# Kernel optimization log

Measured on AMD Instinct MI355X. Metric: run time of the kernel, lower is better.

The kernel has to match this reference:

```python
import jax, jax.numpy as jnp
import numpy as np

# NF4 codebook (bitsandbytes nf4 data type, 16 levels)
NF4_TABLE = np.array([
    -1.0, -0.6961928009986877, -0.5250730514526367, -0.39491748809814453,
    -0.28444138169288635, -0.18477343022823334, -0.09105003625154495, 0.0,
    0.07958029955625534, 0.16093020141124725, 0.24611230194568634,
    0.33791524171829224, 0.44070982933044434, 0.5626170039176941,
    0.7229568362236023, 1.0], dtype=np.float32)

BLOCKSIZE = 64
SCALING = 32.0 / 16.0  # lora_alpha / r


def setup_inputs() -> dict:
    key = jax.random.key(0)
    k1, k2, k3, k4, k5 = jax.random.split(key, 5)
    tokens, in_f, out_f, r = 256, 4096, 11008, 16
    x = jax.random.normal(k1, (tokens, in_f), dtype=jnp.float32)
    q_codes = jax.random.randint(k2, (out_f, in_f), 0, 16, dtype=jnp.int32)
    absmax = jax.random.uniform(k3, (out_f, in_f // BLOCKSIZE), dtype=jnp.float32)
    lora_A = jax.random.normal(k4, (r, in_f), dtype=jnp.float32) * (1.0 / np.sqrt(in_f))
    lora_B = jax.random.normal(k5, (out_f, r), dtype=jnp.float32) * 0.02
    return {"x": x, "q_codes": q_codes, "absmax": absmax,
            "lora_A": lora_A, "lora_B": lora_B}


def reference(x, q_codes, absmax, lora_A, lora_B):
    out_f, in_f = q_codes.shape
    nf4 = jnp.asarray(NF4_TABLE, dtype=x.dtype)
    # Dequantize: codebook lookup, then per-block absmax scale.
    W = nf4[q_codes].reshape(out_f, in_f // BLOCKSIZE, BLOCKSIZE)
    W = (W * absmax[:, :, None]).reshape(out_f, in_f)  # [out_f, in_f]
    # Base 4-bit linear (no bias in bnb Linear4bit default here).
    base = x @ W.T  # [tokens, out_f]
    # LoRA path: dropout p=0 is identity in eval; scaling = alpha/r.
    lora = (x @ lora_A.T) @ lora_B.T  # [tokens, r] -> [tokens, out_f]
    return base + lora * jnp.asarray(SCALING, dtype=x.dtype)
```

## Files before the change

kernel.cpp:

```cpp
#include <hip/hip_runtime.h>
#include <hip/hip_fp16.h>

typedef unsigned int uint;
typedef unsigned short ushort;

typedef __attribute__((ext_vector_type(8))) _Float16 f16x8;
typedef __attribute__((ext_vector_type(4))) float f32x4;

#define TOK 256
#define OUTF 11008
#define INF 4096
#define BM 256
#define BN 64
#define NT2 172
#define NWT 11008

__device__ __constant__ float NF4_TBL[16] = {
    -1.0f, -0.6961928009986877f, -0.5250730514526367f, -0.39491748809814453f,
    -0.28444138169288635f, -0.18477343022823334f, -0.09105003625154495f, 0.0f,
    0.07958029955625534f, 0.16093020141124725f, 0.24611230194568634f,
    0.33791524171829224f, 0.44070982933044434f, 0.5626170039176941f,
    0.7229568362236023f, 1.0f};

__device__ __forceinline__ ushort f2h(float f) {
  return __half_as_ushort(__float2half(f));
}

__device__ __forceinline__ float nf4v(int c, int tbits) {
  return __int_as_float(__builtin_amdgcn_ds_bpermute(c << 2, tbits));
}

__device__ __forceinline__ uint2 dq4(int4 c, __half2 ax2, int tbits) {
  __half2 h0 = __floats2half2_rn(nf4v(c.x, tbits), nf4v(c.y, tbits));
  __half2 h1 = __floats2half2_rn(nf4v(c.z, tbits), nf4v(c.w, tbits));
  h0 = __hmul2(h0, ax2);
  h1 = __hmul2(h1, ax2);
  union { __half2 h[2]; uint2 u; } r;
  r.h[0] = h0; r.h[1] = h1;
  return r.u;
}

__global__ __launch_bounds__(256)
void prep_kernel(const int* __restrict__ qc, const float* __restrict__ am,
                 uint4* __restrict__ wf4, const float* __restrict__ x,
                 uint4* __restrict__ xf4, const float4* __restrict__ lB4,
                 ushort4* __restrict__ lBh4) {
  const int tid = threadIdx.x;
  if (blockIdx.x < NWT) {
    const int b = blockIdx.x;
    const int g = b >> 6, kb = b & 63;
    const int r = tid >> 2;
    const int c = tid & 3;
    const int n = g * 64 + r;
    const int tbits = __float_as_int(NF4_TBL[tid & 15]);
    const __half2 ax2 = __float2half2_rn(am[(size_t)n * 64 + kb]);
    const int4* src = (const int4*)(qc + (size_t)n * INF + kb * 64 + c * 16);
    int4 q0 = src[0], q1 = src[1], q2 = src[2], q3 = src[3];
    uint2 d0 = dq4(q0, ax2, tbits), d1 = dq4(q1, ax2, tbits);
    uint2 d2 = dq4(q2, ax2, tbits), d3 = dq4(q3, ax2, tbits);
    const int rlo = r & 15, nt = r >> 4;
    const int i8a = c * 2, i8b = c * 2 + 1;
    uint4* dst = wf4 + (size_t)b * 512;
    dst[((i8a & 3) * 16 + rlo) * 8 + (i8a >> 2) * 4 + nt] = (uint4){d0.x, d0.y, d1.x, d1.y};
    dst[((i8b & 3) * 16 + rlo) * 8 + (i8b >> 2) * 4 + nt] = (uint4){d2.x, d2.y, d3.x, d3.y};
  } else {
    const int stride = 256 * 256;
    const int t0 = (blockIdx.x - NWT) * 256 + tid;
    for (int f = t0; f < TOK * INF / 8; f += stride) {
      int l = f & 63;
      int rlo = l & 15, chunk = l >> 4;
      int ms = (f >> 6) & 7;
      int mt = ms >> 1, ks2 = ms & 1;
      int w = (f >> 9) & 3;
      int kb = f >> 11;
      int m = w * 64 + mt * 16 + rlo;
      int k0 = kb * 64 + (ks2 * 4 + chunk) * 8;
      const float4* src = (const float4*)(x + (size_t)m * INF + k0);
      float4 v0 = src[0], v1 = src[1];
      union { ushort4 h[2]; uint4 u; } pk;
      pk.h[0].x = f2h(v0.x); pk.h[0].y = f2h(v0.y); pk.h[0].z = f2h(v0.z); pk.h[0].w = f2h(v0.w);
      pk.h[1].x = f2h(v1.x); pk.h[1].y = f2h(v1.y); pk.h[1].z = f2h(v1.z); pk.h[1].w = f2h(v1.w);
      xf4[f] = pk.u;
    }
    for (int i = t0; i < OUTF * 16; i += stride) {
      int n = i >> 4, jq = i & 15;
      ushort4 o = {0, 0, 0, 0};
      if (jq < 4) {
        float4 v = lB4[n * 4 + jq];
        o.x = f2h(v.x); o.y = f2h(v.y); o.z = f2h(v.z); o.w = f2h(v.w);
      }
      lBh4[i] = o;
    }
  }
}

__global__ __launch_bounds__(1024)
void xa_kernel(const float* __restrict__ x, const float* __restrict__ lA,
               ushort* __restrict__ xa2) {
  const int m = blockIdx.x;
  const int t = threadIdx.x;
  const float4* x4 = (const float4*)(x + (size_t)m * INF);
  const float4* lA4 = (const float4*)lA;
  float4 xv = x4[t];
  float acc[16];
#pragma unroll
  for (int j = 0; j < 16; ++j) {
    float4 a = lA4[j * (INF / 4) + t];
    acc[j] = xv.x * a.x + xv.y * a.y + xv.z * a.z + xv.w * a.w;
  }
#pragma unroll
  for (int j = 0; j < 16; ++j)
#pragma unroll
    for (int s = 32; s > 0; s >>= 1) acc[j] += __shfl_xor(acc[j], s, 64);
  __shared__ float red[16][16];
  const int w = t >> 6, l = t & 63;
  if (l == 0) {
#pragma unroll
    for (int j = 0; j < 16; ++j) red[w][j] = acc[j];
  }
  __syncthreads();
  if (t < 64) {
    ushort v = 0;
    if (t < 16) {
      float s = 0.f;
#pragma unroll
      for (int w2 = 0; w2 < 16; ++w2) s += red[w2][t];
      v = f2h(2.0f * s);
    }
    xa2[m * 64 + t] = v;
  }
}

__global__ __launch_bounds__(256, 2)
void gemm_kernel(const ushort* __restrict__ wf, const ushort* __restrict__ xf,
                 const ushort* __restrict__ lBh, const ushort* __restrict__ xa2,
                 float* __restrict__ dest32, ushort* __restrict__ dest16,
                 int nst, int fp16out) {
  const int tid = threadIdx.x;
  const int w = tid >> 6;
  const int l = tid & 63;
  const int chunk = l >> 4;
  const int rlo = l & 15;
  const int split = blockIdx.x / NT2;
  const int ntile = blockIdx.x - split * NT2;
  const int n0 = ntile * BN;
  const int kb0 = split * nst;

  f32x4 acc[4][4];
#pragma unroll
  for (int mt = 0; mt < 4; ++mt)
#pragma unroll
    for (int nt = 0; nt < 4; ++nt) acc[mt][nt] = (f32x4){0.f, 0.f, 0.f, 0.f};

  auto loadA = [&](f16x8 ar[8], int kb) {
    const ushort* base = xf + ((size_t)kb * 4 + w) * 4096 + l * 8;
#pragma unroll
    for (int i = 0; i < 8; ++i) ar[i] = *(const f16x8*)(base + i * 512);
  };
  auto loadB = [&](f16x8 br[8], int kb) {
    const ushort* base = wf + (size_t)(ntile * 64 + kb) * 4096 + l * 64;
#pragma unroll
    for (int f = 0; f < 8; ++f) br[f] = *(const f16x8*)(base + f * 8);
  };
  auto compute = [&](f16x8 ar[8], f16x8 br[8]) {
    __builtin_amdgcn_s_setprio(1);
#pragma unroll
    for (int ks2 = 0; ks2 < 2; ++ks2)
#pragma unroll
      for (int mt = 0; mt < 4; ++mt)
#pragma unroll
        for (int nt = 0; nt < 4; ++nt)
          acc[mt][nt] = __builtin_amdgcn_mfma_f32_16x16x32_f16(
              ar[mt * 2 + ks2], br[ks2 * 4 + nt], acc[mt][nt], 0, 0, 0);
    __builtin_amdgcn_s_setprio(0);
  };

  f16x8 aA[8], bA[8], aB[8], bB[8];
  loadB(bA, kb0);
  loadA(aA, kb0);
  loadB(bB, kb0 + 1);
  loadA(aB, kb0 + 1);

  for (int s = 0; s < nst; s += 2) {
    compute(aA, bA);
    if (s + 2 < nst) { loadB(bA, kb0 + s + 2); loadA(aA, kb0 + s + 2); }
    compute(aB, bB);
    if (s + 3 < nst) { loadB(bB, kb0 + s + 3); loadA(aB, kb0 + s + 3); }
  }

  if (split == 0) {
    f16x8 a_l[4], b_l[4];
#pragma unroll
    for (int mt = 0; mt < 4; ++mt)
      a_l[mt] = *(const f16x8*)(xa2 + (size_t)(w * 64 + mt * 16 + rlo) * 64 + chunk * 8);
#pragma unroll
    for (int nt = 0; nt < 4; ++nt)
      b_l[nt] = *(const f16x8*)(lBh + (size_t)(n0 + nt * 16 + rlo) * 64 + chunk * 8);
#pragma unroll
    for (int mt = 0; mt < 4; ++mt)
#pragma unroll
      for (int nt = 0; nt < 4; ++nt)
        acc[mt][nt] = __builtin_amdgcn_mfma_f32_16x16x32_f16(a_l[mt], b_l[nt], acc[mt][nt], 0, 0, 0);
  }

  if (fp16out) {
    ushort* dst = dest16 + (size_t)split * TOK * OUTF;
#pragma unroll
    for (int mt = 0; mt < 4; ++mt) {
#pragma unroll
      for (int nt = 0; nt < 4; ++nt) {
        int c = n0 + nt * 16 + rlo;
#pragma unroll
        for (int r = 0; r < 4; ++r) {
          int row = w * 64 + mt * 16 + chunk * 4 + r;
          dst[(size_t)row * OUTF + c] = f2h(acc[mt][nt][r]);
        }
      }
    }
  } else {
    float* dst = dest32;
#pragma unroll
    for (int mt = 0; mt < 4; ++mt) {
#pragma unroll
      for (int nt = 0; nt < 4; ++nt) {
        int c = n0 + nt * 16 + rlo;
#pragma unroll
        for (int r = 0; r < 4; ++r) {
          int row = w * 64 + mt * 16 + chunk * 4 + r;
          dst[(size_t)row * OUTF + c] = acc[mt][nt][r];
        }
      }
    }
  }
}

__global__ void reduce_kernel(const uint4* __restrict__ part, float4* __restrict__ out,
                              int ks) {
  const int QN8 = TOK * OUTF / 8;
  int i = blockIdx.x * blockDim.x + threadIdx.x;
  if (i < QN8) {
    float s0 = 0.f, s1 = 0.f, s2 = 0.f, s3 = 0.f, s4 = 0.f, s5 = 0.f, s6 = 0.f, s7 = 0.f;
    for (int sp = 0; sp < ks; ++sp) {
      uint4 v = part[(size_t)sp * QN8 + i];
      union { uint u; __half2 h; } a, b, c, d;
      a.u = v.x; b.u = v.y; c.u = v.z; d.u = v.w;
      float2 fa = __half22float2(a.h), fb = __half22float2(b.h);
      float2 fc = __half22float2(c.h), fd = __half22float2(d.h);
      s0 += fa.x; s1 += fa.y; s2 += fb.x; s3 += fb.y;
      s4 += fc.x; s5 += fc.y; s6 += fd.x; s7 += fd.y;
    }
    out[2 * i] = (float4){s0, s1, s2, s3};
    out[2 * i + 1] = (float4){s4, s5, s6, s7};
  }
}

extern "C" void kernel_launch(void* const* d_in, const int* in_sizes, int n_in,
                              void* d_out, int out_size, void* d_ws, size_t ws_size,
                              hipStream_t stream) {
  const float* x = (const float*)d_in[0];
  const int* qc = (const int*)d_in[1];
  const float* am = (const float*)d_in[2];
  const float* lA = (const float*)d_in[3];
  const float* lB = (const float*)d_in[4];
  float* out = (float*)d_out;

  const size_t off_lB = (size_t)TOK * INF * 2;
  const size_t off_xa2 = off_lB + (size_t)OUTF * 64 * 2;
  const size_t off_wf = off_xa2 + (size_t)TOK * 64 * 2;
  const size_t off_part = off_wf + (size_t)NWT * 8192;
  const size_t part_bytes = (size_t)TOK * OUTF * 2;

  ushort* xf = (ushort*)d_ws;
  ushort* lBh = (ushort*)((char*)d_ws + off_lB);
  ushort* xa2 = (ushort*)((char*)d_ws + off_xa2);
  ushort* wf = (ushort*)((char*)d_ws + off_wf);
  ushort* part = (ushort*)((char*)d_ws + off_part);

  int ks = 1;
  if (ws_size >= off_part + 8 * part_bytes) ks = 8;
  else if (ws_size >= off_part + 4 * part_bytes) ks = 4;
  else if (ws_size >= off_part + 2 * part_bytes) ks = 2;
  const int fp16out = (ks > 1) ? 1 : 0;

  prep_kernel<<<NWT + 256, 256, 0, stream>>>(qc, am, (uint4*)wf, x, (uint4*)xf,
                                             (const float4*)lB, (ushort4*)lBh);
  xa_kernel<<<TOK, 1024, 0, stream>>>(x, lA, xa2);
  gemm_kernel<<<NT2 * ks, 256, 0, stream>>>(wf, xf, lBh, xa2, out, part,
                                            64 / ks, fp16out);
  if (ks > 1)
    reduce_kernel<<<(TOK * OUTF / 8 + 255) / 256, 256, 0, stream>>>((const uint4*)part,
                                                                    (float4*)out, ks);
}
```

Before: 359.5 us.

## Fuse NF4 dequantization into GEMM and drop the fp16 weight buffer

Removes the separate pass that dequantized NF4 codes into a pre-laid-out fp16 weight buffer. The GEMM now loads int32 codes and absmax directly and dequantizes with ds_bpermute in registers. Each wave now owns a 16-column strip across all 256 tokens instead of a 64x64 tile. This is meant to avoid writing and re-reading the intermediate weight buffer. In exchange, activation fragments are re-read from global/L2 by every wave and dequantization ALU work sits inside the MFMA loop.

```diff
diff --git a/kernel.cpp b/kernel.cpp
--- a/kernel.cpp
+++ b/kernel.cpp
@@ -10,10 +10,8 @@
 #define TOK 256
 #define OUTF 11008
 #define INF 4096
-#define BM 256
 #define BN 64
 #define NT2 172
-#define NWT 11008
 
 __device__ __constant__ float NF4_TBL[16] = {
     -1.0f, -0.6961928009986877f, -0.5250730514526367f, -0.39491748809814453f,
@@ -40,57 +38,34 @@
   return r.u;
 }
 
-__global__ __launch_bounds__(256)
-void prep_kernel(const int* __restrict__ qc, const float* __restrict__ am,
-                 uint4* __restrict__ wf4, const float* __restrict__ x,
-                 uint4* __restrict__ xf4, const float4* __restrict__ lB4,
-                 ushort4* __restrict__ lBh4) {
-  const int tid = threadIdx.x;
-  if (blockIdx.x < NWT) {
-    const int b = blockIdx.x;
-    const int g = b >> 6, kb = b & 63;
-    const int r = tid >> 2;
-    const int c = tid & 3;
-    const int n = g * 64 + r;
-    const int tbits = __float_as_int(NF4_TBL[tid & 15]);
-    const __half2 ax2 = __float2half2_rn(am[(size_t)n * 64 + kb]);
-    const int4* src = (const int4*)(qc + (size_t)n * INF + kb * 64 + c * 16);
-    int4 q0 = src[0], q1 = src[1], q2 = src[2], q3 = src[3];
-    uint2 d0 = dq4(q0, ax2, tbits), d1 = dq4(q1, ax2, tbits);
-    uint2 d2 = dq4(q2, ax2, tbits), d3 = dq4(q3, ax2, tbits);
-    const int rlo = r & 15, nt = r >> 4;
-    const int i8a = c * 2, i8b = c * 2 + 1;
-    uint4* dst = wf4 + (size_t)b * 512;
-    dst[((i8a & 3) * 16 + rlo) * 8 + (i8a >> 2) * 4 + nt] = (uint4){d0.x, d0.y, d1.x, d1.y};
-    dst[((i8b & 3) * 16 + rlo) * 8 + (i8b >> 2) * 4 + nt] = (uint4){d2.x, d2.y, d3.x, d3.y};
-  } else {
-    const int stride = 256 * 256;
-    const int t0 = (blockIdx.x - NWT) * 256 + tid;
-    for (int f = t0; f < TOK * INF / 8; f += stride) {
-      int l = f & 63;
-      int rlo = l & 15, chunk = l >> 4;
-      int ms = (f >> 6) & 7;
-      int mt = ms >> 1, ks2 = ms & 1;
-      int w = (f >> 9) & 3;
-      int kb = f >> 11;
-      int m = w * 64 + mt * 16 + rlo;
-      int k0 = kb * 64 + (ks2 * 4 + chunk) * 8;
-      const float4* src = (const float4*)(x + (size_t)m * INF + k0);
-      float4 v0 = src[0], v1 = src[1];
-      union { ushort4 h[2]; uint4 u; } pk;
-      pk.h[0].x = f2h(v0.x); pk.h[0].y = f2h(v0.y); pk.h[0].z = f2h(v0.z); pk.h[0].w = f2h(v0.w);
-      pk.h[1].x = f2h(v1.x); pk.h[1].y = f2h(v1.y); pk.h[1].z = f2h(v1.z); pk.h[1].w = f2h(v1.w);
-      xf4[f] = pk.u;
-    }
-    for (int i = t0; i < OUTF * 16; i += stride) {
-      int n = i >> 4, jq = i & 15;
-      ushort4 o = {0, 0, 0, 0};
-      if (jq < 4) {
-        float4 v = lB4[n * 4 + jq];
-        o.x = f2h(v.x); o.y = f2h(v.y); o.z = f2h(v.z); o.w = f2h(v.w);
-      }
-      lBh4[i] = o;
-    }
+__global__ void prep_kernel(const float* __restrict__ x, uint4* __restrict__ xf4,
+                            const float4* __restrict__ lB4, ushort4* __restrict__ lBh4) {
+  const int stride = gridDim.x * blockDim.x;
+  const int t0 = blockIdx.x * blockDim.x + threadIdx.x;
+  for (int f = t0; f < TOK * INF / 8; f += stride) {
+    int l = f & 63;
+    int rlo = l & 15, chunk = l >> 4;
+    int ms = (f >> 6) & 7;
+    int mt = ms >> 1, ks2 = ms & 1;
+    int m64 = (f >> 9) & 3;
+    int kb = f >> 11;
+    int m = m64 * 64 + mt * 16 + rlo;
+    int k0 = kb * 64 + (ks2 * 4 + chunk) * 8;
+    const float4* src = (const float4*)(x + (size_t)m * INF + k0);
+    float4 v0 = src[0], v1 = src[1];
+    union { ushort4 h[2]; uint4 u; } pk;
+    pk.h[0].x = f2h(v0.x); pk.h[0].y = f2h(v0.y); pk.h[0].z = f2h(v0.z); pk.h[0].w = f2h(v0.w);
+    pk.h[1].x = f2h(v1.x); pk.h[1].y = f2h(v1.y); pk.h[1].z = f2h(v1.z); pk.h[1].w = f2h(v1.w);
+    xf4[f] = pk.u;
+  }
+  for (int i = t0; i < OUTF * 16; i += stride) {
+    int n = i >> 4, jq = i & 15;
+    ushort4 o = {0, 0, 0, 0};
+    if (jq < 4) {
+      float4 v = lB4[n * 4 + jq];
+      o.x = f2h(v.x); o.y = f2h(v.y); o.z = f2h(v.z); o.w = f2h(v.w);
+    }
+    lBh4[i] = o;
   }
 }
 
@@ -132,10 +107,10 @@
 }
 
 __global__ __launch_bounds__(256, 2)
-void gemm_kernel(const ushort* __restrict__ wf, const ushort* __restrict__ xf,
-                 const ushort* __restrict__ lBh, const ushort* __restrict__ xa2,
-                 float* __restrict__ dest32, ushort* __restrict__ dest16,
-                 int nst, int fp16out) {
+void gemm_kernel(const int* __restrict__ qc, const float* __restrict__ am,
+                 const ushort* __restrict__ xf, const ushort* __restrict__ lBh,
+                 const ushort* __restrict__ xa2, float* __restrict__ dest32,
+                 ushort* __restrict__ dest16, int nst, int fp16out) {
   const int tid = threadIdx.x;
   const int w = tid >> 6;
   const int l = tid & 63;
@@ -143,94 +118,90 @@
   const int rlo = l & 15;
   const int split = blockIdx.x / NT2;
   const int ntile = blockIdx.x - split * NT2;
-  const int n0 = ntile * BN;
+  const int nw0 = ntile * BN + w * 16;
   const int kb0 = split * nst;
-
-  f32x4 acc[4][4];
-#pragma unroll
-  for (int mt = 0; mt < 4; ++mt)
-#pragma unroll
-    for (int nt = 0; nt < 4; ++nt) acc[mt][nt] = (f32x4){0.f, 0.f, 0.f, 0.f};
-
-  auto loadA = [&](f16x8 ar[8], int kb) {
-    const ushort* base = xf + ((size_t)kb * 4 + w) * 4096 + l * 8;
-#pragma unroll
-    for (int i = 0; i < 8; ++i) ar[i] = *(const f16x8*)(base + i * 512);
+  const int nr = nw0 + rlo;
+
+  const int tbits = __float_as_int(NF4_TBL[l & 15]);
+  const int* qrow = qc + (size_t)nr * INF + chunk * 8;
+  const float* arow = am + (size_t)nr * 64;
+
+  f32x4 acc[16];
+#pragma unroll
+  for (int mt = 0; mt < 16; ++mt) acc[mt] = (f32x4){0.f, 0.f, 0.f, 0.f};
+
+  auto loadC = [&](int4 (&c)[4], float& ax, int kb) {
+    const int* p = qrow + kb * 64;
+    c[0] = *(const int4*)(p);
+    c[1] = *(const int4*)(p + 4);
+    c[2] = *(const int4*)(p + 32);
+    c[3] = *(const int4*)(p + 36);
+    ax = arow[kb];
   };
-  auto loadB = [&](f16x8 br[8], int kb) {
-    const ushort* base = wf + (size_t)(ntile * 64 + kb) * 4096 + l * 64;
-#pragma unroll
-    for (int f = 0; f < 8; ++f) br[f] = *(const f16x8*)(base + f * 8);
+  auto dqB = [&](const int4 (&c)[4], float ax, f16x8& b0, f16x8& b1) {
+    __half2 ax2 = __float2half2_rn(ax);
+    union { uint2 u2[2]; f16x8 f; } u0, u1;
+    u0.u2[0] = dq4(c[0], ax2, tbits);
+    u0.u2[1] = dq4(c[1], ax2, tbits);
+    u1.u2[0] = dq4(c[2], ax2, tbits);
+    u1.u2[1] = dq4(c[3], ax2, tbits);
+    b0 = u0.f; b1 = u1.f;
   };
-  auto compute = [&](f16x8 ar[8], f16x8 br[8]) {
+  auto sweep = [&](int kb, f16x8 b0, f16x8 b1) {
     __builtin_amdgcn_s_setprio(1);
 #pragma unroll
-    for (int ks2 = 0; ks2 < 2; ++ks2)
-#pragma unroll
-      for (int mt = 0; mt < 4; ++mt)
-#pragma unroll
-        for (int nt = 0; nt < 4; ++nt)
-          acc[mt][nt] = __builtin_amdgcn_mfma_f32_16x16x32_f16(
-              ar[mt * 2 + ks2], br[ks2 * 4 + nt], acc[mt][nt], 0, 0, 0);
+    for (int mt = 0; mt < 16; ++mt) {
+      const ushort* base =
+          xf + (((size_t)kb * 4 + (mt >> 2)) * 8 + (mt & 3) * 2) * 512 + l * 8;
+      f16x8 a0 = *(const f16x8*)(base);
+      f16x8 a1 = *(const f16x8*)(base + 512);
+      acc[mt] = __builtin_amdgcn_mfma_f32_16x16x32_f16(a0, b0, acc[mt], 0, 0, 0);
+      acc[mt] = __builtin_amdgcn_mfma_f32_16x16x32_f16(a1, b1, acc[mt], 0, 0, 0);
+    }
     __builtin_amdgcn_s_setprio(0);
   };
 
-  f16x8 aA[8], bA[8], aB[8], bB[8];
-  loadB(bA, kb0);
-  loadA(aA, kb0);
-  loadB(bB, kb0 + 1);
-  loadA(aB, kb0 + 1);
+  int4 cA[4], cB[4];
+  float axA, axB;
+  loadC(cA, axA, kb0);
+  if (nst > 1) loadC(cB, axB, kb0 + 1);
 
   for (int s = 0; s < nst; s += 2) {
-    compute(aA, bA);
-    if (s + 2 < nst) { loadB(bA, kb0 + s + 2); loadA(aA, kb0 + s + 2); }
-    compute(aB, bB);
-    if (s + 3 < nst) { loadB(bB, kb0 + s + 3); loadA(aB, kb0 + s + 3); }
+    f16x8 b0, b1;
+    dqB(cA, axA, b0, b1);
+    if (s + 2 < nst) loadC(cA, axA, kb0 + s + 2);
+    sweep(kb0 + s, b0, b1);
+    if (s + 1 < nst) {
+      f16x8 b2, b3;
+      dqB(cB, axB, b2, b3);
+      if (s + 3 < nst) loadC(cB, axB, kb0 + s + 3);
+      sweep(kb0 + s + 1, b2, b3);
+    }
   }
 
   if (split == 0) {
-    f16x8 a_l[4], b_l[4];
-#pragma unroll
-    for (int mt = 0; mt < 4; ++mt)
-      a_l[mt] = *(const f16x8*)(xa2 + (size_t)(w * 64 + mt * 16 + rlo) * 64 + chunk * 8);
-#pragma unroll
-    for (int nt = 0; nt < 4; ++nt)
-      b_l[nt] = *(const f16x8*)(lBh + (size_t)(n0 + nt * 16 + rlo) * 64 + chunk * 8);
-#pragma unroll
-    for (int mt = 0; mt < 4; ++mt)
-#pragma unroll
-      for (int nt = 0; nt < 4; ++nt)
-        acc[mt][nt] = __builtin_amdgcn_mfma_f32_16x16x32_f16(a_l[mt], b_l[nt], acc[mt][nt], 0, 0, 0);
+    f16x8 b_l = *(const f16x8*)(lBh + (size_t)nr * 64 + chunk * 8);
+#pragma unroll
+    for (int mt = 0; mt < 16; ++mt) {
+      f16x8 a_l = *(const f16x8*)(xa2 + (size_t)(mt * 16 + rlo) * 64 + chunk * 8);
+      acc[mt] = __builtin_amdgcn_mfma_f32_16x16x32_f16(a_l, b_l, acc[mt], 0, 0, 0);
+    }
   }
 
   if (fp16out) {
-    ushort* dst = dest16 + (size_t)split * TOK * OUTF;
-#pragma unroll
-    for (int mt = 0; mt < 4; ++mt) {
-#pragma unroll
-      for (int nt = 0; nt < 4; ++nt) {
-        int c = n0 + nt * 16 + rlo;
-#pragma unroll
-        for (int r = 0; r < 4; ++r) {
-          int row = w * 64 + mt * 16 + chunk * 4 + r;
-          dst[(size_t)row * OUTF + c] = f2h(acc[mt][nt][r]);
-        }
-      }
-    }
+    ushort* dst = dest16 + (size_t)split * TOK * OUTF + nr;
+#pragma unroll
+    for (int mt = 0; mt < 16; ++mt)
+#pragma unroll
+      for (int r = 0; r < 4; ++r)
+        dst[(size_t)(mt * 16 + chunk * 4 + r) * OUTF] = f2h(acc[mt][r]);
   } else {
-    float* dst = dest32;
-#pragma unroll
-    for (int mt = 0; mt < 4; ++mt) {
-#pragma unroll
-      for (int nt = 0; nt < 4; ++nt) {
-        int c = n0 + nt * 16 + rlo;
-#pragma unroll
-        for (int r = 0; r < 4; ++r) {
-          int row = w * 64 + mt * 16 + chunk * 4 + r;
-          dst[(size_t)row * OUTF + c] = acc[mt][nt][r];
-        }
-      }
-    }
+    float* dst = dest32 + nr;
+#pragma unroll
+    for (int mt = 0; mt < 16; ++mt)
+#pragma unroll
+      for (int r = 0; r < 4; ++r)
+        dst[(size_t)(mt * 16 + chunk * 4 + r) * OUTF] = acc[mt][r];
   }
 }
 
@@ -266,14 +237,12 @@
 
   const size_t off_lB = (size_t)TOK * INF * 2;
   const size_t off_xa2 = off_lB + (size_t)OUTF * 64 * 2;
-  const size_t off_wf = off_xa2 + (size_t)TOK * 64 * 2;
-  const size_t off_part = off_wf + (size_t)NWT * 8192;
+  const size_t off_part = off_xa2 + (size_t)TOK * 64 * 2;
   const size_t part_bytes = (size_t)TOK * OUTF * 2;
 
   ushort* xf = (ushort*)d_ws;
   ushort* lBh = (ushort*)((char*)d_ws + off_lB);
   ushort* xa2 = (ushort*)((char*)d_ws + off_xa2);
-  ushort* wf = (ushort*)((char*)d_ws + off_wf);
   ushort* part = (ushort*)((char*)d_ws + off_part);
 
   int ks = 1;
@@ -282,10 +251,10 @@
   else if (ws_size >= off_part + 2 * part_bytes) ks = 2;
   const int fp16out = (ks > 1) ? 1 : 0;
 
-  prep_kernel<<<NWT + 256, 256, 0, stream>>>(qc, am, (uint4*)wf, x, (uint4*)xf,
-                                             (const float4*)lB, (ushort4*)lBh);
+  prep_kernel<<<2048, 256, 0, stream>>>(x, (uint4*)xf, (const float4*)lB,
+                                        (ushort4*)lBh);
   xa_kernel<<<TOK, 1024, 0, stream>>>(x, lA, xa2);
-  gemm_kernel<<<NT2 * ks, 256, 0, stream>>>(wf, xf, lBh, xa2, out, part,
+  gemm_kernel<<<NT2 * ks, 256, 0, stream>>>(qc, am, xf, lBh, xa2, out, part,
                                             64 / ks, fp16out);
   if (ks > 1)
     reduce_kernel<<<(TOK * OUTF / 8 + 255) / 256, 256, 0, stream>>>((const uint4*)part,
```

New measurement: 336.3 us. -6.4%, faster.
